# Kernel optimization log

Measured on AMD Instinct MI355X. Metric: run time of the kernel, lower is better.

The kernel has to match this reference:

```python
import jax, jax.numpy as jnp
import numpy as np

N, M, C = 200000, 32, 9
VX, VY = 0.2, 0.2
X_OFF, Y_OFF = 0.1, -39.9  # vx/2 + pc_range[0], vy/2 + pc_range[1]
EPS = 1e-3
UNITS = 16  # 64 // 4 per branch

SPATIO_IDX = np.array([0, 1, 2, 5, 6, 7, 8, 9])
VEL_IDX = np.array([3, 10])
SNR_IDX = np.array([4, 11])
LOGIT_IDX = np.array([12, 13, 14, 15])  # num_classes == 3


def setup_inputs() -> dict:
    key = jax.random.key(0)
    ks = jax.random.split(key, 10)
    features = jax.random.normal(ks[0], (N, M, C), jnp.float32)
    num_points = jax.random.randint(ks[1], (N,), 1, M + 1, jnp.int32)
    coors = jnp.concatenate([
        jnp.zeros((N, 2), jnp.int32),
        jax.random.randint(ks[2], (N, 1), 0, 400, jnp.int32),  # y index
        jax.random.randint(ks[3], (N, 1), 0, 352, jnp.int32),  # x index
    ], axis=1)
    w1 = jax.random.normal(ks[4], (UNITS, 8), jnp.float32) * 0.2
    w2 = jax.random.normal(ks[5], (UNITS, 2), jnp.float32) * 0.2
    w3 = jax.random.normal(ks[6], (UNITS, 2), jnp.float32) * 0.2
    w4 = jax.random.normal(ks[7], (UNITS, 4), jnp.float32) * 0.2
    gamma = 1.0 + 0.1 * jax.random.normal(ks[8], (4, UNITS), jnp.float32)
    beta = 0.1 * jax.random.normal(ks[9], (4, UNITS), jnp.float32)
    return {"features": features, "w1": w1, "w2": w2, "w3": w3, "w4": w4,
            "gamma": gamma, "beta": beta, "num_points": num_points, "coors": coors}


def _branch(x, w, g, b):
    # tiny linear (no bias) + BN1d in training mode (stats over N and M)
    y = jnp.einsum('nmc,uc->nmu', x, w)
    mu = y.mean(axis=(0, 1))
    var = y.var(axis=(0, 1))  # biased, matching torch BN normalization
    return (y - mu) * jax.lax.rsqrt(var + EPS) * g + b


def reference(features, w1, w2, w3, w4, gamma, beta, num_points, coors):
    dtype = features.dtype
    npf = num_points.astype(dtype)[:, None, None]  # (N,1,1)

    xyz = features[:, :, :3]
    f_cluster = xyz - xyz.sum(axis=1, keepdims=True) / npf  # (N,M,3)

    cx = coors[:, 3].astype(dtype)[:, None] * VX + X_OFF
    cy = coors[:, 2].astype(dtype)[:, None] * VY + Y_OFF
    f_center = jnp.stack([features[:, :, 0] - cx,
                          features[:, :, 1] - cy], axis=-1)  # (N,M,2)

    vs = features[:, :, 3:5]
    vs_center = vs - vs.sum(axis=1, keepdims=True) / npf  # (N,M,2)

    # legacy=True: f_center aliases features[:, :, :2], so raw cols 0,1 get overwritten
    raw_mod = jnp.concatenate([f_center, features[:, :, 2:]], axis=-1)  # (N,M,9)
    feat = jnp.concatenate([raw_mod, f_cluster, f_center, vs_center], axis=-1)  # (N,M,16)

    mask = (jnp.arange(M)[None, :] < num_points[:, None]).astype(dtype)[:, :, None]
    feat = feat * mask

    x = jnp.concatenate([
        _branch(feat[:, :, SPATIO_IDX], w1, gamma[0], beta[0]),
        _branch(feat[:, :, VEL_IDX],    w2, gamma[1], beta[1]),
        _branch(feat[:, :, SNR_IDX],    w3, gamma[2], beta[2]),
        _branch(feat[:, :, LOGIT_IDX],  w4, gamma[3], beta[3]),
    ], axis=-1)  # (N,M,64)
    x = jax.nn.relu(x)
    return x.max(axis=1)  # max over points, then squeeze of (N,1,64) -> (N,64)
```

## Files before the change

### kernel.cpp

```cpp
#include <hip/hip_runtime.h>
#include <math.h>
#include <stdint.h>


typedef unsigned short u16_t;
typedef __bf16 bf16x8 __attribute__((ext_vector_type(8)));
typedef float floatx16 __attribute__((ext_vector_type(16)));

#define N_P     200000
#define NCHUNK  25000
#define CNT_TOT 6400000.0

__device__ __forceinline__ float bf2f(u16_t u) {
  return __builtin_bit_cast(float, ((unsigned)u) << 16);
}
__device__ __forceinline__ u16_t f2bf(float f) {
  unsigned u = __builtin_bit_cast(unsigned, f);
  u += 0x7FFFu + ((u >> 16) & 1u);
  return (u16_t)(u >> 16);
}
__device__ __forceinline__ unsigned pack_h2(float a, float b) {
  unsigned short ua = __builtin_bit_cast(unsigned short, (_Float16)a);
  unsigned short ub = __builtin_bit_cast(unsigned short, (_Float16)b);
  return (unsigned)ua | ((unsigned)ub << 16);
}
__device__ __forceinline__ float h2lo(unsigned u) {
  return (float)__builtin_bit_cast(_Float16, (unsigned short)(u & 0xFFFFu));
}
__device__ __forceinline__ float h2hi(unsigned u) {
  return (float)__builtin_bit_cast(_Float16, (unsigned short)(u >> 16));
}

template<bool BF16>
__device__ __forceinline__ float ldval(const void* p, size_t i) {
  if constexpr (BF16) return bf2f(((const u16_t*)p)[i]);
  else                return ((const float*)p)[i];
}

struct Pairs { int pi[52]; int pj[52]; int pa[52]; int pb[52]; };
constexpr Pairs makePairs() {
  Pairs P{};
  int n = 0;
  const int L0[8] = {0, 1, 2, 5, 6, 7, 8, 9};
  for (int a = 0; a < 8; ++a)
    for (int b = a; b < 8; ++b) { P.pi[n]=L0[a]; P.pj[n]=L0[b]; P.pa[n]=a; P.pb[n]=b; ++n; }
  const int L1[2] = {3, 10};
  for (int a = 0; a < 2; ++a)
    for (int b = a; b < 2; ++b) { P.pi[n]=L1[a]; P.pj[n]=L1[b]; P.pa[n]=a; P.pb[n]=b; ++n; }
  const int L2[2] = {4, 11};
  for (int a = 0; a < 2; ++a)
    for (int b = a; b < 2; ++b) { P.pi[n]=L2[a]; P.pj[n]=L2[b]; P.pa[n]=a; P.pb[n]=b; ++n; }
  const int L3[4] = {12, 13, 14, 15};
  for (int a = 0; a < 4; ++a)
    for (int b = a; b < 4; ++b) { P.pi[n]=L3[a]; P.pj[n]=L3[b]; P.pa[n]=a; P.pb[n]=b; ++n; }
  return P;
}
constexpr Pairs PT = makePairs();

__global__ void k_detect(const u16_t* __restrict__ f, int* __restrict__ flag) {
  int tid = threadIdx.x;
  int cnt = 0;
  for (int i = 0; i < 4; ++i) {
    unsigned v = f[(size_t)(tid * 4 + i) * 2];
    unsigned e = (v >> 7) & 0xFF;
    cnt += (e >= 100 && e <= 140) ? 1 : 0;
  }
  for (int s = 1; s < 64; s <<= 1) cnt += __shfl_xor(cnt, s);
  if (tid == 0) *flag = (cnt >= 160) ? 1 : 0;
}

template<bool BF16>
__device__ __forceinline__ void derive_feat(
    const void* __restrict__ feats, const int* __restrict__ nump,
    const int* __restrict__ coors, int p, int m, float* feat) {
  size_t base = ((size_t)p * 32 + m) * 9;
  float r[9];
#pragma unroll
  for (int c = 0; c < 9; ++c) r[c] = ldval<BF16>(feats, base + c);
  float sx = r[0], sy = r[1], sz = r[2], svx = r[3], svy = r[4];
#pragma unroll
  for (int sft = 1; sft < 32; sft <<= 1) {
    sx  += __shfl_xor(sx,  sft);
    sy  += __shfl_xor(sy,  sft);
    sz  += __shfl_xor(sz,  sft);
    svx += __shfl_xor(svx, sft);
    svy += __shfl_xor(svy, sft);
  }
  int np = nump[p];
  float inv = 1.0f / (float)np;
  float cx = (float)coors[p * 4 + 3] * 0.2f + 0.1f;
  float cy = (float)coors[p * 4 + 2] * 0.2f - 39.9f;
  feat[0] = r[0] - cx;
  feat[1] = r[1] - cy;
  feat[2] = r[2]; feat[3] = r[3]; feat[4] = r[4];
  feat[5] = r[5]; feat[6] = r[6]; feat[7] = r[7]; feat[8] = r[8];
  feat[9]  = r[0] - sx * inv;
  feat[10] = r[1] - sy * inv;
  feat[11] = r[2] - sz * inv;
  feat[12] = feat[0];
  feat[13] = feat[1];
  feat[14] = r[3] - svx * inv;
  feat[15] = r[4] - svy * inv;
  if (m >= np) {
#pragma unroll
    for (int c = 0; c < 16; ++c) feat[c] = 0.0f;
  }
}

template<bool BF16>
__device__ __forceinline__ float wval(int u, int c,
    const void* w1, const void* w2, const void* w3, const void* w4) {
  int b = u >> 4, k = u & 15;
  if (b == 0) {
    int k2 = (c <= 2) ? c : ((c >= 5 && c <= 9) ? c - 2 : -1);
    return (k2 >= 0) ? ldval<BF16>(w1, k * 8 + k2) : 0.0f;
  } else if (b == 1) {
    if (c == 3)  return ldval<BF16>(w2, k * 2 + 0);
    if (c == 10) return ldval<BF16>(w2, k * 2 + 1);
    return 0.0f;
  } else if (b == 2) {
    if (c == 4)  return ldval<BF16>(w3, k * 2 + 0);
    if (c == 11) return ldval<BF16>(w3, k * 2 + 1);
    return 0.0f;
  }
  if (c >= 12) return ldval<BF16>(w4, k * 4 + (c - 12));
  return 0.0f;
}

template<bool BF16>
__device__ __forceinline__ void pack_frags(int u,
    const void* w1, const void* w2, const void* w3, const void* w4,
    uint4* wsB0hi, uint4* wsB0lo, uint4* wsB1hi, uint4* wsB1lo) {
  int n = u & 31;
  u16_t h0[8], l0[8], h1[8], l1[8];
#pragma unroll
  for (int j = 0; j < 8; ++j) {
    int c = ((u >> 5) << 3) + j;
    float v0 = wval<BF16>(n,      c, w1, w2, w3, w4);
    float v1 = wval<BF16>(n + 32, c, w1, w2, w3, w4);
    h0[j] = f2bf(v0); h1[j] = f2bf(v1);
    l0[j] = BF16 ? (u16_t)0 : f2bf(v0 - bf2f(h0[j]));
    l1[j] = BF16 ? (u16_t)0 : f2bf(v1 - bf2f(h1[j]));
  }
  uint4 a0, a1, c0, c1;
  a0.x = h0[0] | ((unsigned)h0[1] << 16); a0.y = h0[2] | ((unsigned)h0[3] << 16);
  a0.z = h0[4] | ((unsigned)h0[5] << 16); a0.w = h0[6] | ((unsigned)h0[7] << 16);
  c0.x = l0[0] | ((unsigned)l0[1] << 16); c0.y = l0[2] | ((unsigned)l0[3] << 16);
  c0.z = l0[4] | ((unsigned)l0[5] << 16); c0.w = l0[6] | ((unsigned)l0[7] << 16);
  a1.x = h1[0] | ((unsigned)h1[1] << 16); a1.y = h1[2] | ((unsigned)h1[3] << 16);
  a1.z = h1[4] | ((unsigned)h1[5] << 16); a1.w = h1[6] | ((unsigned)h1[7] << 16);
  c1.x = l1[0] | ((unsigned)l1[1] << 16); c1.y = l1[2] | ((unsigned)l1[3] << 16);
  c1.z = l1[4] | ((unsigned)l1[5] << 16); c1.w = l1[6] | ((unsigned)l1[7] << 16);
  wsB0hi[u] = a0; wsB0lo[u] = c0;
  wsB1hi[u] = a1; wsB1lo[u] = c1;
}


template<bool BF16>
__global__ void k_prep(const void* __restrict__ w1, const void* __restrict__ w2,
                       const void* __restrict__ w3, const void* __restrict__ w4,
                       const int* __restrict__ flag,
                       uint4* __restrict__ wsB0hi, uint4* __restrict__ wsB0lo,
                       uint4* __restrict__ wsB1hi, uint4* __restrict__ wsB1lo) {
  if (*flag != (BF16 ? 1 : 0)) return;
  pack_frags<BF16>(threadIdx.x, w1, w2, w3, w4, wsB0hi, wsB0lo, wsB1hi, wsB1lo);
}

template<bool BF16>
__global__ __launch_bounds__(256) void k_fused(
    const void* __restrict__ feats, const int* __restrict__ nump,
    const int* __restrict__ coors, const int* __restrict__ flag,
    const uint4* __restrict__ wsB0hi, const uint4* __restrict__ wsB0lo,
    const uint4* __restrict__ wsB1hi, const uint4* __restrict__ wsB1lo,
    unsigned* __restrict__ mm, float* __restrict__ part, int g1) {
  if (*flag != (BF16 ? 1 : 0)) return;
  constexpr int TILE = 8 * 32 * 3;
  __shared__ uint4 featL[(BF16 ? 1 : 2) * TILE];
  __shared__ float red[4][128];
  int tid = threadIdx.x;
  int wave = tid >> 6, lane = tid & 63;
  int pp = (lane >> 5) & 1, m = lane & 31;

  bf16x8 B0h = __builtin_bit_cast(bf16x8, wsB0hi[lane]);
  bf16x8 B1h = __builtin_bit_cast(bf16x8, wsB1hi[lane]);
  bf16x8 B0l, B1l;
  if constexpr (!BF16) {
    B0l = __builtin_bit_cast(bf16x8, wsB0lo[lane]);
    B1l = __builtin_bit_cast(bf16x8, wsB1lo[lane]);
  }
  floatx16 z;
#pragma unroll
  for (int i = 0; i < 16; ++i) z[i] = 0.0f;

  float sA0 = 0.0f, sQ0 = 0.0f, sA1 = 0.0f, sQ1 = 0.0f;

  for (int chunk = blockIdx.x; chunk < NCHUNK; chunk += g1) {
    int wp = wave * 2 + pp;
    int p  = chunk * 8 + wp;
    float feat[16];
    derive_feat<BF16>(feats, nump, coors, p, m, feat);

    unsigned pkh[8], pkl[8];
#pragma unroll
    for (int j = 0; j < 8; ++j) {
      float a0 = feat[2 * j], a1 = feat[2 * j + 1];
      u16_t h0 = f2bf(a0), h1 = f2bf(a1);
      pkh[j] = (unsigned)h0 | ((unsigned)h1 << 16);
      if constexpr (!BF16) {
        u16_t q0 = f2bf(a0 - bf2f(h0)), q1 = f2bf(a1 - bf2f(h1));
        pkl[j] = (unsigned)q0 | ((unsigned)q1 << 16);
      }
    }
    uint4 v;
    v.x = pkh[0]; v.y = pkh[1]; v.z = pkh[2]; v.w = pkh[3];
    featL[(wp * 32 + m) * 3 + 0] = v;
    v.x = pkh[4]; v.y = pkh[5]; v.z = pkh[6]; v.w = pkh[7];
    featL[(wp * 32 + m) * 3 + 1] = v;
    if constexpr (!BF16) {
      v.x = pkl[0]; v.y = pkl[1]; v.z = pkl[2]; v.w = pkl[3];
      featL[TILE + (wp * 32 + m) * 3 + 0] = v;
      v.x = pkl[4]; v.y = pkl[5]; v.z = pkl[6]; v.w = pkl[7];
      featL[TILE + (wp * 32 + m) * 3 + 1] = v;
    }

#pragma unroll
    for (int q = 0; q < 2; ++q) {
      int wq = wave * 2 + q;
      int pq = chunk * 8 + wq;
      int ridx = (wq * 32 + (lane & 31)) * 3 + (lane >> 5);
      bf16x8 Ah = __builtin_bit_cast(bf16x8, featL[ridx]);
      floatx16 d0, d1;
      if constexpr (BF16) {
        d0 = __builtin_amdgcn_mfma_f32_32x32x16_bf16(Ah, B0h, z, 0, 0, 0);
        d1 = __builtin_amdgcn_mfma_f32_32x32x16_bf16(Ah, B1h, z, 0, 0, 0);
      } else {
        bf16x8 Al = __builtin_bit_cast(bf16x8, featL[TILE + ridx]);
        d0 = __builtin_amdgcn_mfma_f32_32x32x16_bf16(Al, B0h, z, 0, 0, 0);
        d0 = __builtin_amdgcn_mfma_f32_32x32x16_bf16(Ah, B0l, d0, 0, 0, 0);
        d0 = __builtin_amdgcn_mfma_f32_32x32x16_bf16(Ah, B0h, d0, 0, 0, 0);
        d1 = __builtin_amdgcn_mfma_f32_32x32x16_bf16(Al, B1h, z, 0, 0, 0);
        d1 = __builtin_amdgcn_mfma_f32_32x32x16_bf16(Ah, B1l, d1, 0, 0, 0);
        d1 = __builtin_amdgcn_mfma_f32_32x32x16_bf16(Ah, B1h, d1, 0, 0, 0);
      }
      float mx0 = d0[0], mn0 = d0[0], l0s = d0[0], l0q = d0[0] * d0[0];
      float mx1 = d1[0], mn1 = d1[0], l1s = d1[0], l1q = d1[0] * d1[0];
#pragma unroll
      for (int r = 1; r < 16; ++r) {
        float a = d0[r], b = d1[r];
        mx0 = fmaxf(mx0, a); mn0 = fminf(mn0, a);
        l0s += a; l0q = fmaf(a, a, l0q);
        mx1 = fmaxf(mx1, b); mn1 = fminf(mn1, b);
        l1s += b; l1q = fmaf(b, b, l1q);
      }
      sA0 += l0s; sQ0 += l0q; sA1 += l1s; sQ1 += l1q;
      mx0 = fmaxf(mx0, __shfl_xor(mx0, 32));
      mn0 = fminf(mn0, __shfl_xor(mn0, 32));
      mx1 = fmaxf(mx1, __shfl_xor(mx1, 32));
      mn1 = fminf(mn1, __shfl_xor(mn1, 32));
      unsigned outw = (lane < 32) ? pack_h2(mx0, mn0) : pack_h2(mx1, mn1);
      mm[(size_t)pq * 64 + lane] = outw;
    }
  }

  sA0 += __shfl_xor(sA0, 32); sQ0 += __shfl_xor(sQ0, 32);
  sA1 += __shfl_xor(sA1, 32); sQ1 += __shfl_xor(sQ1, 32);
  if (lane < 32) {
    red[wave][lane]      = sA0;
    red[wave][32 + lane] = sA1;
    red[wave][64 + lane] = sQ0;
    red[wave][96 + lane] = sQ1;
  }
  __syncthreads();
  if (tid < 128)
    part[(size_t)tid * g1 + blockIdx.x] =
        red[0][tid] + red[1][tid] + red[2][tid] + red[3][tid];
}

__global__ void k_reduce2(const float* __restrict__ part,
                          double* __restrict__ mom, int g1) {
  int j = blockIdx.x, tid = threadIdx.x;
  double s = 0.0;
  for (int b = tid; b < g1; b += 256) s += (double)part[(size_t)j * g1 + b];
  __shared__ double red[256];
  red[tid] = s;
  __syncthreads();
  for (int off = 128; off; off >>= 1) {
    if (tid < off) red[tid] += red[tid + off];
    __syncthreads();
  }
  if (tid == 0) mom[j] = red[0];
}

template<bool BF16>
__global__ void k_fin2(const double* __restrict__ mom,
                       const void* __restrict__ gamma, const void* __restrict__ beta,
                       const int* __restrict__ flag,
                       float* __restrict__ wsS, float* __restrict__ wsT) {
  if (*flag != (BF16 ? 1 : 0)) return;
  int u = threadIdx.x;
  double mu  = mom[u] / CNT_TOT;
  double var = mom[64 + u] / CNT_TOT - mu * mu;
  float g  = ldval<BF16>(gamma, u);
  float be = ldval<BF16>(beta, u);
  float S = (float)(1.0 / sqrt(var + 1e-3)) * g;
  float T = be - (float)mu * S;
  wsS[u] = S;
  wsT[u] = T;
}

template<bool BF16>
__global__ __launch_bounds__(256) void k_out(
    const uint4* __restrict__ mm4, const float* __restrict__ wsS,
    const float* __restrict__ wsT, const int* __restrict__ flag,
    void* __restrict__ outv) {
  if (*flag != (BF16 ? 1 : 0)) return;
  __shared__ float sS[64], sT[64];
  int tid = threadIdx.x;
  if (tid < 64) { sS[tid] = wsS[tid]; sT[tid] = wsT[tid]; }
  __syncthreads();
  const int total = N_P * 16;
  for (int i = blockIdx.x * 256 + tid; i < total; i += gridDim.x * 256) {
    uint4 v = mm4[i];
    unsigned w[4] = {v.x, v.y, v.z, v.w};
    int u0 = (i & 15) * 4;
    float o[4];
#pragma unroll
    for (int j = 0; j < 4; ++j) {
      float mx = h2lo(w[j]), mn = h2hi(w[j]);
      float S = sS[u0 + j], T = sT[u0 + j];
      float zz = (S > 0.0f) ? fmaf(S, mx, T) : fmaf(S, mn, T);
      o[j] = fmaxf(zz, 0.0f);
    }
    if constexpr (BF16) {
      uint2 r;
      r.x = (unsigned)f2bf(o[0]) | ((unsigned)f2bf(o[1]) << 16);
      r.y = (unsigned)f2bf(o[2]) | ((unsigned)f2bf(o[3]) << 16);
      ((uint2*)outv)[i] = r;
    } else {
      float4 f;
      f.x = o[0]; f.y = o[1]; f.z = o[2]; f.w = o[3];
      ((float4*)outv)[i] = f;
    }
  }
}


template<bool BF16>
__global__ void k_moments(const void* __restrict__ feats,
                          const int* __restrict__ nump,
                          const int* __restrict__ coors,
                          const int* __restrict__ flag,
                          float* __restrict__ part, int g1) {
  if (*flag != (BF16 ? 1 : 0)) return;
  int tid = threadIdx.x;
  int wave = tid >> 6, lane = tid & 63;
  int pp = (lane >> 5) & 1, m = lane & 31;
  float acc[68];
#pragma unroll
  for (int i = 0; i < 68; ++i) acc[i] = 0.0f;

  for (int chunk = blockIdx.x; chunk < NCHUNK; chunk += g1) {
    int p = chunk * 8 + wave * 2 + pp;
    float feat[16];
    derive_feat<BF16>(feats, nump, coors, p, m, feat);
#pragma unroll
    for (int c = 0; c < 16; ++c) acc[c] += feat[c];
#pragma unroll
    for (int t = 0; t < 52; ++t)
      acc[16 + t] = fmaf(feat[PT.pi[t]], feat[PT.pj[t]], acc[16 + t]);
  }

#pragma unroll
  for (int k = 0; k < 68; ++k) {
    float v = acc[k];
#pragma unroll
    for (int sft = 1; sft < 64; sft <<= 1) v += __shfl_xor(v, sft);
    acc[k] = v;
  }
  __shared__ float red[4][68];
  if (lane == 0) {
#pragma unroll
    for (int k = 0; k < 68; ++k) red[wave][k] = acc[k];
  }
  __syncthreads();
  if (tid < 68) {
    float t = red[0][tid] + red[1][tid] + red[2][tid] + red[3][tid];
    part[(size_t)tid * g1 + blockIdx.x] = t;
  }
}

__global__ void k_reduce(const float* __restrict__ part,
                         float* __restrict__ mom, int g1) {
  int j = blockIdx.x, tid = threadIdx.x;
  float s = 0.0f;
  for (int b = tid; b < g1; b += 256) s += part[(size_t)j * g1 + b];
  __shared__ float red[256];
  red[tid] = s;
  __syncthreads();
  for (int off = 128; off; off >>= 1) {
    if (tid < off) red[tid] += red[tid + off];
    __syncthreads();
  }
  if (tid == 0) mom[j] = red[0];
}

template<bool BF16>
__global__ void k_finalize(const float* __restrict__ mom,
    const void* __restrict__ w1, const void* __restrict__ w2,
    const void* __restrict__ w3, const void* __restrict__ w4,
    const void* __restrict__ gamma, const void* __restrict__ beta,
    const int* __restrict__ flag,
    float* __restrict__ wsS, float* __restrict__ wsT,
    uint4* __restrict__ wsB0hi, uint4* __restrict__ wsB0lo,
    uint4* __restrict__ wsB1hi, uint4* __restrict__ wsB1lo) {
  if (*flag != (BF16 ? 1 : 0)) return;
  int u = threadIdx.x;
  const int CHOFF[4] = {0, 8, 10, 12};
  const int CCNT[4]  = {8, 2, 2, 4};
  const int LCH[16]  = {0,1,2,5,6,7,8,9, 3,10, 4,11, 12,13,14,15};
  const int PBASE[4] = {0, 36, 39, 42};
  const int PCNTB[4] = {36, 3, 3, 10};

  int b = u >> 4, k = u & 15;
  const void* wsrc = (b == 0) ? w1 : (b == 1) ? w2 : (b == 2) ? w3 : w4;
  int cc = CCNT[b];
  float  w[8];
  double mf[8];
  for (int i = 0; i < 8; ++i) { w[i] = 0.0f; mf[i] = 0.0; }
  for (int i = 0; i < cc; ++i) {
    w[i]  = ldval<BF16>(wsrc, k * cc + i);
    mf[i] = (double)mom[LCH[CHOFF[b] + i]] / CNT_TOT;
  }
  double mu = 0.0;
  for (int i = 0; i < cc; ++i) mu += (double)w[i] * mf[i];
  double var = 0.0;
  for (int t = 0; t < PCNTB[b]; ++t) {
    int idx = PBASE[b] + t;
    int a = PT.pa[idx], b2 = PT.pb[idx];
    double e2  = (double)mom[16 + idx] / CNT_TOT;
    double cov = e2 - mf[a] * mf[b2];
    var += ((a == b2) ? 1.0 : 2.0) * (double)w[a] * (double)w[b2] * cov;
  }
  float g  = ldval<BF16>(gamma, u);
  float be = ldval<BF16>(beta, u);
  float S = (float)(1.0 / sqrt(var + 1e-3)) * g;
  float T = be - (float)mu * S;
  wsS[u] = S;
  wsT[u] = T;

  pack_frags<BF16>(u, w1, w2, w3, w4, wsB0hi, wsB0lo, wsB1hi, wsB1lo);
}

template<bool BF16>
__global__ __launch_bounds__(256) void k_main(
    const void* __restrict__ feats, const int* __restrict__ nump,
    const int* __restrict__ coors, const int* __restrict__ flag,
    const float* __restrict__ wsS, const float* __restrict__ wsT,
    const uint4* __restrict__ wsB0hi, const uint4* __restrict__ wsB0lo,
    const uint4* __restrict__ wsB1hi, const uint4* __restrict__ wsB1lo,
    void* __restrict__ outv) {
  if (*flag != (BF16 ? 1 : 0)) return;
  constexpr int TILE = 8 * 32 * 3;
  __shared__ uint4 featL[(BF16 ? 1 : 2) * TILE];
  int tid = threadIdx.x;
  int wave = tid >> 6, lane = tid & 63;
  int pp = (lane >> 5) & 1, m = lane & 31;

  bf16x8 B0h = __builtin_bit_cast(bf16x8, wsB0hi[lane]);
  bf16x8 B1h = __builtin_bit_cast(bf16x8, wsB1hi[lane]);
  bf16x8 B0l, B1l;
  if constexpr (!BF16) {
    B0l = __builtin_bit_cast(bf16x8, wsB0lo[lane]);
    B1l = __builtin_bit_cast(bf16x8, wsB1lo[lane]);
  }
  int ucol = lane & 31;
  float s0 = wsS[ucol],      t0 = wsT[ucol];
  float s1 = wsS[ucol + 32], t1 = wsT[ucol + 32];

  int wp = wave * 2 + pp;
  int p  = blockIdx.x * 8 + wp;
  float feat[16];
  derive_feat<BF16>(feats, nump, coors, p, m, feat);

  unsigned pkh[8], pkl[8];
#pragma unroll
  for (int j = 0; j < 8; ++j) {
    float a0 = feat[2 * j], a1 = feat[2 * j + 1];
    u16_t h0 = f2bf(a0), h1 = f2bf(a1);
    pkh[j] = (unsigned)h0 | ((unsigned)h1 << 16);
    if constexpr (!BF16) {
      u16_t q0 = f2bf(a0 - bf2f(h0)), q1 = f2bf(a1 - bf2f(h1));
      pkl[j] = (unsigned)q0 | ((unsigned)q1 << 16);
    }
  }
  uint4 v;
  v.x = pkh[0]; v.y = pkh[1]; v.z = pkh[2]; v.w = pkh[3];
  featL[(wp * 32 + m) * 3 + 0] = v;
  v.x = pkh[4]; v.y = pkh[5]; v.z = pkh[6]; v.w = pkh[7];
  featL[(wp * 32 + m) * 3 + 1] = v;
  if constexpr (!BF16) {
    v.x = pkl[0]; v.y = pkl[1]; v.z = pkl[2]; v.w = pkl[3];
    featL[TILE + (wp * 32 + m) * 3 + 0] = v;
    v.x = pkl[4]; v.y = pkl[5]; v.z = pkl[6]; v.w = pkl[7];
    featL[TILE + (wp * 32 + m) * 3 + 1] = v;
  }
  __syncthreads();

  floatx16 z;
#pragma unroll
  for (int i = 0; i < 16; ++i) z[i] = 0.0f;

#pragma unroll
  for (int q = 0; q < 2; ++q) {
    int wq = wave * 2 + q;
    int ridx = (wq * 32 + (lane & 31)) * 3 + (lane >> 5);
    bf16x8 Ah = __builtin_bit_cast(bf16x8, featL[ridx]);
    floatx16 d0, d1;
    if constexpr (BF16) {
      d0 = __builtin_amdgcn_mfma_f32_32x32x16_bf16(Ah, B0h, z, 0, 0, 0);
      d1 = __builtin_amdgcn_mfma_f32_32x32x16_bf16(Ah, B1h, z, 0, 0, 0);
    } else {
      bf16x8 Al = __builtin_bit_cast(bf16x8, featL[TILE + ridx]);
      d0 = __builtin_amdgcn_mfma_f32_32x32x16_bf16(Al, B0h, z, 0, 0, 0);
      d0 = __builtin_amdgcn_mfma_f32_32x32x16_bf16(Ah, B0l, d0, 0, 0, 0);
      d0 = __builtin_amdgcn_mfma_f32_32x32x16_bf16(Ah, B0h, d0, 0, 0, 0);
      d1 = __builtin_amdgcn_mfma_f32_32x32x16_bf16(Al, B1h, z, 0, 0, 0);
      d1 = __builtin_amdgcn_mfma_f32_32x32x16_bf16(Ah, B1l, d1, 0, 0, 0);
      d1 = __builtin_amdgcn_mfma_f32_32x32x16_bf16(Ah, B1h, d1, 0, 0, 0);
    }
    float mx0 = fmaf(d0[0], s0, t0);
    float mx1 = fmaf(d1[0], s1, t1);
#pragma unroll
    for (int r = 1; r < 16; ++r) {
      mx0 = fmaxf(mx0, fmaf(d0[r], s0, t0));
      mx1 = fmaxf(mx1, fmaf(d1[r], s1, t1));
    }
    mx0 = fmaxf(mx0, __shfl_xor(mx0, 32));
    mx1 = fmaxf(mx1, __shfl_xor(mx1, 32));
    mx0 = fmaxf(mx0, 0.0f);
    mx1 = fmaxf(mx1, 0.0f);
    float val = (lane < 32) ? mx0 : mx1;
    size_t oidx = (size_t)(blockIdx.x * 8 + wq) * 64 + lane;
    if constexpr (BF16) ((u16_t*)outv)[oidx] = f2bf(val);
    else                ((float*)outv)[oidx] = val;
  }
}

extern "C" void kernel_launch(void* const* d_in, const int* in_sizes, int n_in,
                              void* d_out, int out_size, void* d_ws, size_t ws_size,
                              hipStream_t stream) {
  (void)in_sizes; (void)n_in; (void)out_size;
  const void* feats = d_in[0];
  const void* w1    = d_in[1];
  const void* w2    = d_in[2];
  const void* w3    = d_in[3];
  const void* w4    = d_in[4];
  const void* gamma = d_in[5];
  const void* beta  = d_in[6];
  const int*  nump  = (const int*)d_in[7];
  const int*  coors = (const int*)d_in[8];

  char* ws = (char*)d_ws;
  int*   flag   = (int*)(ws + 0);
  float* wsS    = (float*)(ws + 64);
  float* wsT    = (float*)(ws + 320);
  uint4* wsB0hi = (uint4*)(ws + 576);
  uint4* wsB0lo = (uint4*)(ws + 1600);
  uint4* wsB1hi = (uint4*)(ws + 2624);
  uint4* wsB1lo = (uint4*)(ws + 3648);

  const int g1f = 1024;
  double*   mom2  = (double*)(ws + 4672);
  float*    part2 = (float*)(ws + 5696);
  unsigned* mm    = (unsigned*)(ws + 529984);
  size_t need_fused = 529984ull + (size_t)N_P * 64ull * 4ull;

  if (ws_size >= need_fused) {
    k_detect<<<1, 64, 0, stream>>>((const u16_t*)feats, flag);
    k_prep<true ><<<1, 64, 0, stream>>>(w1, w2, w3, w4, flag, wsB0hi, wsB0lo, wsB1hi, wsB1lo);
    k_prep<false><<<1, 64, 0, stream>>>(w1, w2, w3, w4, flag, wsB0hi, wsB0lo, wsB1hi, wsB1lo);
    k_fused<true ><<<g1f, 256, 0, stream>>>(feats, nump, coors, flag,
                                            wsB0hi, wsB0lo, wsB1hi, wsB1lo, mm, part2, g1f);
    k_fused<false><<<g1f, 256, 0, stream>>>(feats, nump, coors, flag,
                                            wsB0hi, wsB0lo, wsB1hi, wsB1lo, mm, part2, g1f);
    k_reduce2<<<128, 256, 0, stream>>>(part2, mom2, g1f);
    k_fin2<true ><<<1, 64, 0, stream>>>(mom2, gamma, beta, flag, wsS, wsT);
    k_fin2<false><<<1, 64, 0, stream>>>(mom2, gamma, beta, flag, wsS, wsT);
    k_out<true ><<<2048, 256, 0, stream>>>((const uint4*)mm, wsS, wsT, flag, d_out);
    k_out<false><<<2048, 256, 0, stream>>>((const uint4*)mm, wsS, wsT, flag, d_out);
    return;
  }

  float* mom  = (float*)(ws + 4672);
  float* part = (float*)(ws + 5120);

  int g1 = 1024;
  size_t need = 5120 + (size_t)68 * (size_t)g1 * 4;
  if (need > ws_size) {
    size_t avail = (ws_size > 5120) ? (ws_size - 5120) : 0;
    g1 = (int)(avail / (68 * 4));
    if (g1 > 1024) g1 = 1024;
    if (g1 < 8) g1 = 8;
  }

  k_detect<<<1, 64, 0, stream>>>((const u16_t*)feats, flag);
  k_moments<true ><<<g1, 256, 0, stream>>>(feats, nump, coors, flag, part, g1);
  k_moments<false><<<g1, 256, 0, stream>>>(feats, nump, coors, flag, part, g1);
  k_reduce<<<68, 256, 0, stream>>>(part, mom, g1);
  k_finalize<true ><<<1, 64, 0, stream>>>(mom, w1, w2, w3, w4, gamma, beta, flag,
                                          wsS, wsT, wsB0hi, wsB0lo, wsB1hi, wsB1lo);
  k_finalize<false><<<1, 64, 0, stream>>>(mom, w1, w2, w3, w4, gamma, beta, flag,
                                          wsS, wsT, wsB0hi, wsB0lo, wsB1hi, wsB1lo);
  k_main<true ><<<N_P / 8, 256, 0, stream>>>(feats, nump, coors, flag, wsS, wsT,
                                             wsB0hi, wsB0lo, wsB1hi, wsB1lo, d_out);
  k_main<false><<<N_P / 8, 256, 0, stream>>>(feats, nump, coors, flag, wsS, wsT,
                                             wsB0hi, wsB0lo, wsB1hi, wsB1lo, d_out);
}
```

Measured before the change: 405.1 us.

## Fold gamma sign into weights, store only max as fp16, drop LDS staging

The sign of gamma is folded into the packed MFMA weights, so only the per-point max (not max and min) needs to be kept, and the intermediate buffer becomes one fp16 per channel instead of a packed max/min pair. The LDS tile staging of the A fragments is replaced with cross-lane shuffles, and feature loads are vectorised. The grid grows to 2048 blocks with launch bounds of 4, and the output kernel handles 8 channels per thread. These changes cut intermediate memory traffic and LDS use. The per-block partial buffer layout changes, and the fused path now depends on the sign folding being mirrored consistently in both finalize paths.

```diff
diff --git a/kernel.cpp b/kernel.cpp
--- a/kernel.cpp
+++ b/kernel.cpp
@@ -5,6 +5,7 @@
 
 typedef unsigned short u16_t;
 typedef __bf16 bf16x8 __attribute__((ext_vector_type(8)));
+typedef __bf16 bf16x2_t __attribute__((ext_vector_type(2)));
 typedef float floatx16 __attribute__((ext_vector_type(16)));
 
 #define N_P     200000
@@ -19,10 +20,9 @@
   u += 0x7FFFu + ((u >> 16) & 1u);
   return (u16_t)(u >> 16);
 }
-__device__ __forceinline__ unsigned pack_h2(float a, float b) {
-  unsigned short ua = __builtin_bit_cast(unsigned short, (_Float16)a);
-  unsigned short ub = __builtin_bit_cast(unsigned short, (_Float16)b);
-  return (unsigned)ua | ((unsigned)ub << 16);
+__device__ __forceinline__ unsigned packbf(float a, float b) {
+  bf16x2_t v; v[0] = (__bf16)a; v[1] = (__bf16)b;
+  return __builtin_bit_cast(unsigned, v);
 }
 __device__ __forceinline__ float h2lo(unsigned u) {
   return (float)__builtin_bit_cast(_Float16, (unsigned short)(u & 0xFFFFu));
@@ -75,8 +75,18 @@
     const int* __restrict__ coors, int p, int m, float* feat) {
   size_t base = ((size_t)p * 32 + m) * 9;
   float r[9];
-#pragma unroll
-  for (int c = 0; c < 9; ++c) r[c] = ldval<BF16>(feats, base + c);
+  if constexpr (BF16) {
+#pragma unroll
+    for (int c = 0; c < 9; ++c) r[c] = bf2f(((const u16_t*)feats)[base + c]);
+  } else {
+    const float* fp = (const float*)feats + base;
+    float v0[4], v1[4];
+    __builtin_memcpy(v0, fp, 16);
+    __builtin_memcpy(v1, fp + 4, 16);
+    r[0]=v0[0]; r[1]=v0[1]; r[2]=v0[2]; r[3]=v0[3];
+    r[4]=v1[0]; r[5]=v1[1]; r[6]=v1[2]; r[7]=v1[3];
+    r[8]=fp[8];
+  }
   float sx = r[0], sy = r[1], sz = r[2], svx = r[3], svy = r[4];
 #pragma unroll
   for (int sft = 1; sft < 32; sft <<= 1) {
@@ -130,14 +140,19 @@
 template<bool BF16>
 __device__ __forceinline__ void pack_frags(int u,
     const void* w1, const void* w2, const void* w3, const void* w4,
+    const void* gamma,
     uint4* wsB0hi, uint4* wsB0lo, uint4* wsB1hi, uint4* wsB1lo) {
   int n = u & 31;
+  float g0 = ldval<BF16>(gamma, n);
+  float g1 = ldval<BF16>(gamma, n + 32);
+  float sg0 = (g0 < 0.0f) ? -1.0f : 1.0f;
+  float sg1 = (g1 < 0.0f) ? -1.0f : 1.0f;
   u16_t h0[8], l0[8], h1[8], l1[8];
 #pragma unroll
   for (int j = 0; j < 8; ++j) {
     int c = ((u >> 5) << 3) + j;
-    float v0 = wval<BF16>(n,      c, w1, w2, w3, w4);
-    float v1 = wval<BF16>(n + 32, c, w1, w2, w3, w4);
+    float v0 = wval<BF16>(n,      c, w1, w2, w3, w4) * sg0;
+    float v1 = wval<BF16>(n + 32, c, w1, w2, w3, w4) * sg1;
     h0[j] = f2bf(v0); h1[j] = f2bf(v1);
     l0[j] = BF16 ? (u16_t)0 : f2bf(v0 - bf2f(h0[j]));
     l1[j] = BF16 ? (u16_t)0 : f2bf(v1 - bf2f(h1[j]));
@@ -159,27 +174,28 @@
 template<bool BF16>
 __global__ void k_prep(const void* __restrict__ w1, const void* __restrict__ w2,
                        const void* __restrict__ w3, const void* __restrict__ w4,
+                       const void* __restrict__ gamma,
                        const int* __restrict__ flag,
                        uint4* __restrict__ wsB0hi, uint4* __restrict__ wsB0lo,
                        uint4* __restrict__ wsB1hi, uint4* __restrict__ wsB1lo) {
   if (*flag != (BF16 ? 1 : 0)) return;
-  pack_frags<BF16>(threadIdx.x, w1, w2, w3, w4, wsB0hi, wsB0lo, wsB1hi, wsB1lo);
-}
-
-template<bool BF16>
-__global__ __launch_bounds__(256) void k_fused(
+  pack_frags<BF16>(threadIdx.x, w1, w2, w3, w4, gamma,
+                   wsB0hi, wsB0lo, wsB1hi, wsB1lo);
+}
+
+template<bool BF16>
+__global__ __launch_bounds__(256, 4) void k_fused(
     const void* __restrict__ feats, const int* __restrict__ nump,
     const int* __restrict__ coors, const int* __restrict__ flag,
     const uint4* __restrict__ wsB0hi, const uint4* __restrict__ wsB0lo,
     const uint4* __restrict__ wsB1hi, const uint4* __restrict__ wsB1lo,
-    unsigned* __restrict__ mm, float* __restrict__ part, int g1) {
+    u16_t* __restrict__ mm, float* __restrict__ part, int g1) {
   if (*flag != (BF16 ? 1 : 0)) return;
-  constexpr int TILE = 8 * 32 * 3;
-  __shared__ uint4 featL[(BF16 ? 1 : 2) * TILE];
   __shared__ float red[4][128];
   int tid = threadIdx.x;
   int wave = tid >> 6, lane = tid & 63;
   int pp = (lane >> 5) & 1, m = lane & 31;
+  bool lo = (lane < 32);
 
   bf16x8 B0h = __builtin_bit_cast(bf16x8, wsB0hi[lane]);
   bf16x8 B1h = __builtin_bit_cast(bf16x8, wsB1hi[lane]);
@@ -195,46 +211,51 @@
   float sA0 = 0.0f, sQ0 = 0.0f, sA1 = 0.0f, sQ1 = 0.0f;
 
   for (int chunk = blockIdx.x; chunk < NCHUNK; chunk += g1) {
-    int wp = wave * 2 + pp;
-    int p  = chunk * 8 + wp;
+    int p = chunk * 8 + wave * 2 + pp;
     float feat[16];
     derive_feat<BF16>(feats, nump, coors, p, m, feat);
 
-    unsigned pkh[8], pkl[8];
+    unsigned H[8], L[8];
 #pragma unroll
     for (int j = 0; j < 8; ++j) {
       float a0 = feat[2 * j], a1 = feat[2 * j + 1];
-      u16_t h0 = f2bf(a0), h1 = f2bf(a1);
-      pkh[j] = (unsigned)h0 | ((unsigned)h1 << 16);
+      __bf16 h0 = (__bf16)a0, h1 = (__bf16)a1;
+      bf16x2_t hv; hv[0] = h0; hv[1] = h1;
+      H[j] = __builtin_bit_cast(unsigned, hv);
       if constexpr (!BF16) {
-        u16_t q0 = f2bf(a0 - bf2f(h0)), q1 = f2bf(a1 - bf2f(h1));
-        pkl[j] = (unsigned)q0 | ((unsigned)q1 << 16);
+        L[j] = packbf(a0 - (float)h0, a1 - (float)h1);
       }
     }
-    uint4 v;
-    v.x = pkh[0]; v.y = pkh[1]; v.z = pkh[2]; v.w = pkh[3];
-    featL[(wp * 32 + m) * 3 + 0] = v;
-    v.x = pkh[4]; v.y = pkh[5]; v.z = pkh[6]; v.w = pkh[7];
-    featL[(wp * 32 + m) * 3 + 1] = v;
-    if constexpr (!BF16) {
-      v.x = pkl[0]; v.y = pkl[1]; v.z = pkl[2]; v.w = pkl[3];
-      featL[TILE + (wp * 32 + m) * 3 + 0] = v;
-      v.x = pkl[4]; v.y = pkl[5]; v.z = pkl[6]; v.w = pkl[7];
-      featL[TILE + (wp * 32 + m) * 3 + 1] = v;
+    unsigned Q0[4], Q1[4], Q0l[4], Q1l[4];
+#pragma unroll
+    for (int j = 0; j < 4; ++j) {
+      unsigned pre = lo ? H[4 + j] : H[j];
+      unsigned t = (unsigned)__shfl_xor((int)pre, 32);
+      Q0[j] = lo ? H[j] : t;
+      Q1[j] = lo ? t : H[4 + j];
+      if constexpr (!BF16) {
+        unsigned prel = lo ? L[4 + j] : L[j];
+        unsigned tl = (unsigned)__shfl_xor((int)prel, 32);
+        Q0l[j] = lo ? L[j] : tl;
+        Q1l[j] = lo ? tl : L[4 + j];
+      }
     }
 
 #pragma unroll
     for (int q = 0; q < 2; ++q) {
-      int wq = wave * 2 + q;
-      int pq = chunk * 8 + wq;
-      int ridx = (wq * 32 + (lane & 31)) * 3 + (lane >> 5);
-      bf16x8 Ah = __builtin_bit_cast(bf16x8, featL[ridx]);
+      uint4 ah;
+      if (q == 0) { ah.x = Q0[0]; ah.y = Q0[1]; ah.z = Q0[2]; ah.w = Q0[3]; }
+      else        { ah.x = Q1[0]; ah.y = Q1[1]; ah.z = Q1[2]; ah.w = Q1[3]; }
+      bf16x8 Ah = __builtin_bit_cast(bf16x8, ah);
       floatx16 d0, d1;
       if constexpr (BF16) {
         d0 = __builtin_amdgcn_mfma_f32_32x32x16_bf16(Ah, B0h, z, 0, 0, 0);
         d1 = __builtin_amdgcn_mfma_f32_32x32x16_bf16(Ah, B1h, z, 0, 0, 0);
       } else {
-        bf16x8 Al = __builtin_bit_cast(bf16x8, featL[TILE + ridx]);
+        uint4 al;
+        if (q == 0) { al.x = Q0l[0]; al.y = Q0l[1]; al.z = Q0l[2]; al.w = Q0l[3]; }
+        else        { al.x = Q1l[0]; al.y = Q1l[1]; al.z = Q1l[2]; al.w = Q1l[3]; }
+        bf16x8 Al = __builtin_bit_cast(bf16x8, al);
         d0 = __builtin_amdgcn_mfma_f32_32x32x16_bf16(Al, B0h, z, 0, 0, 0);
         d0 = __builtin_amdgcn_mfma_f32_32x32x16_bf16(Ah, B0l, d0, 0, 0, 0);
         d0 = __builtin_amdgcn_mfma_f32_32x32x16_bf16(Ah, B0h, d0, 0, 0, 0);
@@ -242,23 +263,31 @@
         d1 = __builtin_amdgcn_mfma_f32_32x32x16_bf16(Ah, B1l, d1, 0, 0, 0);
         d1 = __builtin_amdgcn_mfma_f32_32x32x16_bf16(Ah, B1h, d1, 0, 0, 0);
       }
-      float mx0 = d0[0], mn0 = d0[0], l0s = d0[0], l0q = d0[0] * d0[0];
-      float mx1 = d1[0], mn1 = d1[0], l1s = d1[0], l1q = d1[0] * d1[0];
-#pragma unroll
-      for (int r = 1; r < 16; ++r) {
-        float a = d0[r], b = d1[r];
-        mx0 = fmaxf(mx0, a); mn0 = fminf(mn0, a);
-        l0s += a; l0q = fmaf(a, a, l0q);
-        mx1 = fmaxf(mx1, b); mn1 = fminf(mn1, b);
-        l1s += b; l1q = fmaf(b, b, l1q);
+      float mx0 = d0[0], mx1 = d1[0];
+      float l0s = d0[0], l1s = d1[0];
+      float l0q = d0[0] * d0[0], l1q = d1[0] * d1[0];
+#pragma unroll
+      for (int r = 1; r < 15; r += 2) {
+        float a = d0[r], a2 = d0[r + 1], b = d1[r], b2 = d1[r + 1];
+        mx0 = fmaxf(fmaxf(mx0, a), a2);
+        mx1 = fmaxf(fmaxf(mx1, b), b2);
+        l0s += a + a2;  l1s += b + b2;
+        l0q = fmaf(a, a, l0q);  l0q = fmaf(a2, a2, l0q);
+        l1q = fmaf(b, b, l1q);  l1q = fmaf(b2, b2, l1q);
+      }
+      {
+        float a = d0[15], b = d1[15];
+        mx0 = fmaxf(mx0, a); mx1 = fmaxf(mx1, b);
+        l0s += a; l1s += b;
+        l0q = fmaf(a, a, l0q); l1q = fmaf(b, b, l1q);
       }
       sA0 += l0s; sQ0 += l0q; sA1 += l1s; sQ1 += l1q;
       mx0 = fmaxf(mx0, __shfl_xor(mx0, 32));
-      mn0 = fminf(mn0, __shfl_xor(mn0, 32));
       mx1 = fmaxf(mx1, __shfl_xor(mx1, 32));
-      mn1 = fminf(mn1, __shfl_xor(mn1, 32));
-      unsigned outw = (lane < 32) ? pack_h2(mx0, mn0) : pack_h2(mx1, mn1);
-      mm[(size_t)pq * 64 + lane] = outw;
+      float val = lo ? mx0 : mx1;
+      _Float16 hf = (_Float16)val;
+      int pq = chunk * 8 + wave * 2 + q;
+      mm[(size_t)pq * 64 + lane] = __builtin_bit_cast(u16_t, hf);
     }
   }
 
@@ -302,7 +331,7 @@
   double var = mom[64 + u] / CNT_TOT - mu * mu;
   float g  = ldval<BF16>(gamma, u);
   float be = ldval<BF16>(beta, u);
-  float S = (float)(1.0 / sqrt(var + 1e-3)) * g;
+  float S = (float)(1.0 / sqrt(var + 1e-3)) * fabsf(g);
   float T = be - (float)mu * S;
   wsS[u] = S;
   wsT[u] = T;
@@ -318,28 +347,29 @@
   int tid = threadIdx.x;
   if (tid < 64) { sS[tid] = wsS[tid]; sT[tid] = wsT[tid]; }
   __syncthreads();
-  const int total = N_P * 16;
+  const int total = N_P * 8;
   for (int i = blockIdx.x * 256 + tid; i < total; i += gridDim.x * 256) {
     uint4 v = mm4[i];
     unsigned w[4] = {v.x, v.y, v.z, v.w};
-    int u0 = (i & 15) * 4;
-    float o[4];
+    int u0 = (i & 7) * 8;
+    float o[8];
 #pragma unroll
     for (int j = 0; j < 4; ++j) {
-      float mx = h2lo(w[j]), mn = h2hi(w[j]);
-      float S = sS[u0 + j], T = sT[u0 + j];
-      float zz = (S > 0.0f) ? fmaf(S, mx, T) : fmaf(S, mn, T);
-      o[j] = fmaxf(zz, 0.0f);
+      float mxa = h2lo(w[j]), mxb = h2hi(w[j]);
+      o[2 * j]     = fmaxf(fmaf(sS[u0 + 2 * j],     mxa, sT[u0 + 2 * j]),     0.0f);
+      o[2 * j + 1] = fmaxf(fmaf(sS[u0 + 2 * j + 1], mxb, sT[u0 + 2 * j + 1]), 0.0f);
     }
     if constexpr (BF16) {
-      uint2 r;
-      r.x = (unsigned)f2bf(o[0]) | ((unsigned)f2bf(o[1]) << 16);
-      r.y = (unsigned)f2bf(o[2]) | ((unsigned)f2bf(o[3]) << 16);
-      ((uint2*)outv)[i] = r;
+      uint4 r;
+      r.x = packbf(o[0], o[1]); r.y = packbf(o[2], o[3]);
+      r.z = packbf(o[4], o[5]); r.w = packbf(o[6], o[7]);
+      ((uint4*)outv)[i] = r;
     } else {
-      float4 f;
-      f.x = o[0]; f.y = o[1]; f.z = o[2]; f.w = o[3];
-      ((float4*)outv)[i] = f;
+      float4 f0, f1;
+      f0.x = o[0]; f0.y = o[1]; f0.z = o[2]; f0.w = o[3];
+      f1.x = o[4]; f1.y = o[5]; f1.z = o[6]; f1.w = o[7];
+      ((float4*)outv)[i * 2]     = f0;
+      ((float4*)outv)[i * 2 + 1] = f1;
     }
   }
 }
@@ -445,10 +475,10 @@
   float be = ldval<BF16>(beta, u);
   float S = (float)(1.0 / sqrt(var + 1e-3)) * g;
   float T = be - (float)mu * S;
-  wsS[u] = S;
+  wsS[u] = fabsf(S);
   wsT[u] = T;
 
-  pack_frags<BF16>(u, w1, w2, w3, w4, wsB0hi, wsB0lo, wsB1hi, wsB1lo);
+  pack_frags<BF16>(u, w1, w2, w3, w4, gamma, wsB0hi, wsB0lo, wsB1hi, wsB1lo);
 }
 
 template<bool BF16>
@@ -569,16 +599,18 @@
   uint4* wsB1hi = (uint4*)(ws + 2624);
   uint4* wsB1lo = (uint4*)(ws + 3648);
 
-  const int g1f = 1024;
-  double*   mom2  = (double*)(ws + 4672);
-  float*    part2 = (float*)(ws + 5696);
-  unsigned* mm    = (unsigned*)(ws + 529984);
-  size_t need_fused = 529984ull + (size_t)N_P * 64ull * 4ull;
+  const int g1f = 2048;
+  double* mom2  = (double*)(ws + 4672);
+  float*  part2 = (float*)(ws + 5696);
+  u16_t*  mm    = (u16_t*)(ws + 1054336);
+  size_t need_fused = 1054336ull + (size_t)N_P * 64ull * 2ull;
 
   if (ws_size >= need_fused) {
     k_detect<<<1, 64, 0, stream>>>((const u16_t*)feats, flag);
-    k_prep<true ><<<1, 64, 0, stream>>>(w1, w2, w3, w4, flag, wsB0hi, wsB0lo, wsB1hi, wsB1lo);
-    k_prep<false><<<1, 64, 0, stream>>>(w1, w2, w3, w4, flag, wsB0hi, wsB0lo, wsB1hi, wsB1lo);
+    k_prep<true ><<<1, 64, 0, stream>>>(w1, w2, w3, w4, gamma, flag,
+                                        wsB0hi, wsB0lo, wsB1hi, wsB1lo);
+    k_prep<false><<<1, 64, 0, stream>>>(w1, w2, w3, w4, gamma, flag,
+                                        wsB0hi, wsB0lo, wsB1hi, wsB1lo);
     k_fused<true ><<<g1f, 256, 0, stream>>>(feats, nump, coors, flag,
                                             wsB0hi, wsB0lo, wsB1hi, wsB1lo, mm, part2, g1f);
     k_fused<false><<<g1f, 256, 0, stream>>>(feats, nump, coors, flag,
```

After: 377.9 us. 1.07x faster.
